# Kernel optimization log

Hardware: AMD Instinct MI355X
Metric: run time of the kernel (lower is better)

Reference implementation:

```python
import jax, jax.numpy as jnp
import numpy as np

# Irrep layout: blocks of (multiplicity, l); identical for input and output.
LS = [0, 1, 2, 3]
MULS = [64, 64, 64, 64]
N = 65536
DIM = sum(m * (2 * l + 1) for m, l in zip(MULS, LS))  # 1024
NPATH = len(LS) * len(LS)  # 16 valid (l_out, l_in) paths
MAXM = max(LS)             # max |m| over all paths
NW = sum(mo * mi for mo in MULS for mi in MULS)  # 65536 path weights


def _split_blocks(x):
    """Split flat irrep vector into per-block [n, mul, 2l+1] views."""
    blocks, off = [], 0
    for mul, l in zip(MULS, LS):
        d = mul * (2 * l + 1)
        blocks.append(x[:, off:off + d].reshape(x.shape[0], mul, 2 * l + 1))
        off += d
    return blocks


def setup_inputs() -> dict:
    key = jax.random.key(0)
    k = jax.random.split(key, 5)
    return {
        "x": jax.random.normal(k[0], (N, DIM), jnp.float32),
        "weights": jax.random.normal(k[1], (NW,), jnp.float32) * 0.1,
        "hzero": jax.random.normal(k[2], (NPATH,), jnp.float32),
        "hpos": jax.random.normal(k[3], (NPATH, MAXM), jnp.float32),
        "hneg": jax.random.normal(k[4], (NPATH, MAXM), jnp.float32),
    }


def reference(x, weights, hzero, hpos, hneg):
    xb = _split_blocks(x)
    n = x.shape[0]
    outb = [jnp.zeros((n, mul, 2 * l + 1), x.dtype) for mul, l in zip(MULS, LS)]
    p, off = 0, 0
    for oi, (mo, lo) in enumerate(zip(MULS, LS)):
        for ii, (mi, li) in enumerate(zip(MULS, LS)):
            W = weights[off:off + mo * mi].reshape(mo, mi)
            off += mo * mi
            xi = xb[ii]  # [n, mi, 2*li+1]
            # m = 0 component
            y0 = jnp.einsum('nm,om->no', xi[:, :, li], W) * hzero[p]
            outb[oi] = outb[oi].at[:, :, lo].add(y0)
            # |m| >= 1: O(2)-reduced pos/neg mixing with Wigner-derived couplings
            for m in range(1, min(lo, li) + 1):
                hp, hn = hpos[p, m - 1], hneg[p, m - 1]
                xp, xn = xi[:, :, li + m], xi[:, :, li - m]
                outb[oi] = outb[oi].at[:, :, lo + m].add(
                    jnp.einsum('nm,om->no', hp * xp + hn * xn, W))
                outb[oi] = outb[oi].at[:, :, lo - m].add(
                    jnp.einsum('nm,om->no', hp * xn - hn * xp, W))
            p += 1
    return jnp.concatenate([b.reshape(n, -1) for b in outb], axis=1)
```

## Files before the change

### kernel.cpp

```cpp
#include <hip/hip_runtime.h>


typedef __attribute__((ext_vector_type(8))) short bhalf8_t;
typedef __attribute__((ext_vector_type(4))) float f32x4_t;

#define NROWS 65536
#define DIMV  1024
#define NT    512
#define RPW   32

#define M0_OFF 0
#define M1_OFF 65536
#define M2_OFF 212992
#define M3_OFF 278528
#define M_TOTAL 294912

#define OP 1028

#define XB1_OFF 11520

__device__ __forceinline__ short f2bf(float f) {
    unsigned u = __builtin_bit_cast(unsigned, f);
    u = (u + 0x7FFFu + ((u >> 16) & 1u)) >> 16;
    return (short)u;
}

__global__ __launch_bounds__(256) void build_M(const float* __restrict__ w,
                                               const float* __restrict__ hz,
                                               const float* __restrict__ hp,
                                               const float* __restrict__ hn,
                                               short* __restrict__ M) {
    int idx = blockIdx.x * 256 + threadIdx.x;
    if (idx >= M_TOTAL) return;

    int m, A, B;
    if (idx < M1_OFF)      { m = 0; int lo = idx;            A = lo / 256u; B = lo - A * 256; }
    else if (idx < M2_OFF) { m = 1; int lo = idx - M1_OFF;   A = lo / 384u; B = lo - A * 384; }
    else if (idx < M3_OFF) { m = 2; int lo = idx - M2_OFF;   A = lo / 256u; B = lo - A * 256; }
    else                   { m = 3; int lo = idx - M3_OFF;   A = lo / 128u; B = lo - A * 128; }

    int ob, so, o, ib, si, i;
    if (m == 0) { ob = A >> 6;       so = 0;            o = A & 63;
                  ib = B >> 6;       si = 0;            i = B & 63; }
    else        { ob = (A >> 7) + m; so = (A >> 6) & 1; o = A & 63;
                  ib = (B >> 7) + m; si = (B >> 6) & 1; i = B & 63; }

    int p = ob * 4 + ib;
    float wv = w[p * 4096 + o * 64 + i];
    float coef;
    if (m == 0) {
        coef = hz[p];
    } else {
        float hpv = hp[p * 3 + (m - 1)];
        float hnv = hn[p * 3 + (m - 1)];
        coef = (so == 0) ? ((si == 0) ? hpv : hnv)
                         : ((si == 0) ? -hnv : hpv);
    }
    M[idx] = f2bf(wv * coef);
}

template<int L>
__device__ __forceinline__ void stage_block(const float* __restrict__ x, int rowbase,
                                            short* __restrict__ xb, int tid) {
    constexpr int nch = 2 * L + 1;
    constexpr int d4  = 16 * nch;
    constexpr int RS  = nch * 72;
    constexpr int bo  = 64 * L * L;
#pragma unroll
    for (int e = 0; e < nch; ++e) {
        int id  = e * NT + tid;
        int row = id / d4;
        int cc  = id - row * d4;
        int col = cc * 4;
        const float4 v = *(const float4*)(x + (size_t)(rowbase + row) * DIMV + bo + col);
        short* dst = &xb[row * RS];
        { int ci = col;     int i = ci / nch; int ji = ci - i * nch; dst[ji * 72 + i] = f2bf(v.x); }
        { int ci = col + 1; int i = ci / nch; int ji = ci - i * nch; dst[ji * 72 + i] = f2bf(v.y); }
        { int ci = col + 2; int i = ci / nch; int ji = ci - i * nch; dst[ji * 72 + i] = f2bf(v.z); }
        { int ci = col + 3; int i = ci / nch; int ji = ci - i * nch; dst[ji * 72 + i] = f2bf(v.w); }
    }
}

template<int L>
__device__ __forceinline__ void compute_block(const short* __restrict__ xb,
                                              const short* __restrict__ Mg,
                                              int m, int Wm, int cb, int lr, int q,
                                              f32x4_t acc[8][2]) {
    if (m > L) return;
    constexpr int nch = 2 * L + 1;
    constexpr int RS  = nch * 72;
    const int nsi = (m == 0) ? 1 : 2;
    for (int si = 0; si < nsi; ++si) {
        const int ji    = L + ((si == 0) ? m : -m);
        const int kbase = (m == 0) ? (L << 6) : (((L - m) << 7) + (si << 6));
#pragma unroll
        for (int kk = 0; kk < 2; ++kk) {
            bhalf8_t a[2];
            const int eo = ji * 72 + kk * 32 + q * 8;
#pragma unroll
            for (int r = 0; r < 2; ++r)
                a[r] = *(const bhalf8_t*)&xb[(r * 16 + lr) * RS + eo];
            const int ko = kbase + kk * 32 + q * 8;
#pragma unroll
            for (int c = 0; c < 8; ++c) {
                const bhalf8_t b = *(const bhalf8_t*)&Mg[(cb + c * 16 + lr) * Wm + ko];
#pragma unroll
                for (int r = 0; r < 2; ++r)
                    acc[c][r] = __builtin_amdgcn_mfma_f32_16x16x32_bf16(
                        a[r], b, acc[c][r], 0, 0, 0);
            }
        }
    }
}

__global__ __launch_bounds__(NT, 4) void tp_main(const float* __restrict__ x,
                                                 const short* __restrict__ Mall,
                                                 float* __restrict__ out) {
    __shared__ __align__(16) char smem[16 * OP * 4];
    short* __restrict__ xb0  = (short*)smem;
    short* __restrict__ xb1  = (short*)smem + XB1_OFF;
    float* __restrict__ obuf = (float*)smem;

    const int tid  = threadIdx.x;
    const int lane = tid & 63;
    const int lr   = lane & 15;
    const int q    = lane >> 4;
    const int wv   = tid >> 6;
    const int rowbase = blockIdx.x * RPW;

    int m, cb;
    if      (wv < 2) { m = 0; cb = wv << 7; }
    else if (wv < 5) { m = 1; cb = (wv - 2) << 7; }
    else if (wv < 7) { m = 2; cb = (wv - 5) << 7; }
    else             { m = 3; cb = 0; }
    const int Wm   = (m == 1) ? 384 : ((m == 3) ? 128 : 256);
    const int Moff = (m == 0) ? M0_OFF : (m == 1) ? M1_OFF : (m == 2) ? M2_OFF : M3_OFF;
    const short* __restrict__ Mg = Mall + Moff;

    f32x4_t acc[8][2];
#pragma unroll
    for (int c = 0; c < 8; ++c)
#pragma unroll
        for (int r = 0; r < 2; ++r)
            acc[c][r] = (f32x4_t){0.f, 0.f, 0.f, 0.f};

    stage_block<0>(x, rowbase, xb0, tid);
    __syncthreads();

    stage_block<1>(x, rowbase, xb1, tid);
    compute_block<0>(xb0, Mg, m, Wm, cb, lr, q, acc);
    __syncthreads();

    stage_block<2>(x, rowbase, xb0, tid);
    compute_block<1>(xb1, Mg, m, Wm, cb, lr, q, acc);
    __syncthreads();

    stage_block<3>(x, rowbase, xb1, tid);
    compute_block<2>(xb0, Mg, m, Wm, cb, lr, q, acc);
    __syncthreads();

    compute_block<3>(xb1, Mg, m, Wm, cb, lr, q, acc);
    __syncthreads();

    int origc[8];
#pragma unroll
    for (int c = 0; c < 8; ++c) {
        const int P = cb + c * 16 + lr;
        int ob, o, jo;
        if (m == 0) { ob = P >> 6;       o = P & 63; jo = ob; }
        else        { ob = (P >> 7) + m; o = P & 63;
                      jo = ob + ((((P >> 6) & 1) == 0) ? m : -m); }
        origc[c] = 64 * ob * ob + o * (2 * ob + 1) + jo;
    }

#pragma unroll
    for (int r2 = 0; r2 < 2; ++r2) {
#pragma unroll
        for (int c = 0; c < 8; ++c) {
#pragma unroll
            for (int g = 0; g < 4; ++g)
                obuf[(q * 4 + g) * OP + origc[c]] = acc[c][r2][g];
        }
        __syncthreads();
#pragma unroll
        for (int it = 0; it < 8; ++it) {
            const int j   = it * NT + tid;
            const int row = j >> 8;
            const int c4  = (j & 255) << 2;
            const float4 v = *(const float4*)&obuf[row * OP + c4];
            *(float4*)&out[(size_t)(rowbase + r2 * 16 + row) * DIMV + c4] = v;
        }
        __syncthreads();
    }
}

extern "C" void kernel_launch(void* const* d_in, const int* in_sizes, int n_in,
                              void* d_out, int out_size, void* d_ws, size_t ws_size,
                              hipStream_t stream) {
    const float* x   = (const float*)d_in[0];
    const float* wts = (const float*)d_in[1];
    const float* hz  = (const float*)d_in[2];
    const float* hp  = (const float*)d_in[3];
    const float* hn  = (const float*)d_in[4];
    float* out = (float*)d_out;
    short* M   = (short*)d_ws;

    build_M<<<dim3(M_TOTAL / 256), dim3(256), 0, stream>>>(wts, hz, hp, hn, M);
    tp_main<<<dim3(NROWS / RPW), dim3(NT), 0, stream>>>(x, M, out);
}
```

Baseline: 583.1 us.

## Double rows per block and prefetch x blocks into registers with single LDS buffer

Each block now handles 64 rows instead of 32, so every M fragment loaded from global memory is reused across four MFMA row tiles instead of two. The LDS double buffer is replaced by a single buffer. The next irrep block of x is loaded into registers while the current block computes, then written to LDS after a barrier. This cuts M reloads per row and keeps global loads overlapped with compute. In exchange it doubles the accumulator registers, lowers the occupancy hint from 4 to 2 blocks per CU, adds barriers, and halves the grid size.

After: 612.8 us. +5.1%, slower.

```diff
diff --git a/kernel.cpp b/kernel.cpp
--- a/kernel.cpp
+++ b/kernel.cpp
@@ -7,7 +7,7 @@
 #define NROWS 65536
 #define DIMV  1024
 #define NT    512
-#define RPW   32
+#define RPW   64
 
 #define M0_OFF 0
 #define M1_OFF 65536
@@ -16,8 +16,6 @@
 #define M_TOTAL 294912
 
 #define OP 1028
-
-#define XB1_OFF 11520
 
 __device__ __forceinline__ short f2bf(float f) {
     unsigned u = __builtin_bit_cast(unsigned, f);
@@ -60,24 +58,38 @@
 }
 
 template<int L>
-__device__ __forceinline__ void stage_block(const float* __restrict__ x, int rowbase,
+__device__ __forceinline__ void load_block(const float* __restrict__ x, int rowbase,
+                                           int tid, float4* __restrict__ v) {
+    constexpr int nch = 2 * L + 1;
+    constexpr int d4  = 16 * nch;
+    constexpr int bo  = 64 * L * L;
+#pragma unroll
+    for (int e = 0; e < 2 * nch; ++e) {
+        int id  = e * NT + tid;
+        int row = id / d4;
+        int cc  = id - row * d4;
+        v[e] = *(const float4*)(x + (size_t)(rowbase + row) * DIMV + bo + cc * 4);
+    }
+}
+
+template<int L>
+__device__ __forceinline__ void write_block(const float4* __restrict__ v,
                                             short* __restrict__ xb, int tid) {
     constexpr int nch = 2 * L + 1;
     constexpr int d4  = 16 * nch;
     constexpr int RS  = nch * 72;
-    constexpr int bo  = 64 * L * L;
-#pragma unroll
-    for (int e = 0; e < nch; ++e) {
+#pragma unroll
+    for (int e = 0; e < 2 * nch; ++e) {
         int id  = e * NT + tid;
         int row = id / d4;
         int cc  = id - row * d4;
         int col = cc * 4;
-        const float4 v = *(const float4*)(x + (size_t)(rowbase + row) * DIMV + bo + col);
         short* dst = &xb[row * RS];
-        { int ci = col;     int i = ci / nch; int ji = ci - i * nch; dst[ji * 72 + i] = f2bf(v.x); }
-        { int ci = col + 1; int i = ci / nch; int ji = ci - i * nch; dst[ji * 72 + i] = f2bf(v.y); }
-        { int ci = col + 2; int i = ci / nch; int ji = ci - i * nch; dst[ji * 72 + i] = f2bf(v.z); }
-        { int ci = col + 3; int i = ci / nch; int ji = ci - i * nch; dst[ji * 72 + i] = f2bf(v.w); }
+        const float4 w = v[e];
+        { int ci = col;     int i = ci / nch; int ji = ci - i * nch; dst[ji * 72 + i] = f2bf(w.x); }
+        { int ci = col + 1; int i = ci / nch; int ji = ci - i * nch; dst[ji * 72 + i] = f2bf(w.y); }
+        { int ci = col + 2; int i = ci / nch; int ji = ci - i * nch; dst[ji * 72 + i] = f2bf(w.z); }
+        { int ci = col + 3; int i = ci / nch; int ji = ci - i * nch; dst[ji * 72 + i] = f2bf(w.w); }
     }
 }
 
@@ -85,7 +97,7 @@
 __device__ __forceinline__ void compute_block(const short* __restrict__ xb,
                                               const short* __restrict__ Mg,
                                               int m, int Wm, int cb, int lr, int q,
-                                              f32x4_t acc[8][2]) {
+                                              f32x4_t (&acc)[8][4]) {
     if (m > L) return;
     constexpr int nch = 2 * L + 1;
     constexpr int RS  = nch * 72;
@@ -95,17 +107,17 @@
         const int kbase = (m == 0) ? (L << 6) : (((L - m) << 7) + (si << 6));
 #pragma unroll
         for (int kk = 0; kk < 2; ++kk) {
-            bhalf8_t a[2];
+            bhalf8_t a[4];
             const int eo = ji * 72 + kk * 32 + q * 8;
 #pragma unroll
-            for (int r = 0; r < 2; ++r)
+            for (int r = 0; r < 4; ++r)
                 a[r] = *(const bhalf8_t*)&xb[(r * 16 + lr) * RS + eo];
             const int ko = kbase + kk * 32 + q * 8;
 #pragma unroll
             for (int c = 0; c < 8; ++c) {
                 const bhalf8_t b = *(const bhalf8_t*)&Mg[(cb + c * 16 + lr) * Wm + ko];
 #pragma unroll
-                for (int r = 0; r < 2; ++r)
+                for (int r = 0; r < 4; ++r)
                     acc[c][r] = __builtin_amdgcn_mfma_f32_16x16x32_bf16(
                         a[r], b, acc[c][r], 0, 0, 0);
             }
@@ -113,12 +125,11 @@
     }
 }
 
-__global__ __launch_bounds__(NT, 4) void tp_main(const float* __restrict__ x,
+__global__ __launch_bounds__(NT, 2) void tp_main(const float* __restrict__ x,
                                                  const short* __restrict__ Mall,
                                                  float* __restrict__ out) {
     __shared__ __align__(16) char smem[16 * OP * 4];
-    short* __restrict__ xb0  = (short*)smem;
-    short* __restrict__ xb1  = (short*)smem + XB1_OFF;
+    short* __restrict__ xbuf = (short*)smem;
     float* __restrict__ obuf = (float*)smem;
 
     const int tid  = threadIdx.x;
@@ -137,30 +148,38 @@
     const int Moff = (m == 0) ? M0_OFF : (m == 1) ? M1_OFF : (m == 2) ? M2_OFF : M3_OFF;
     const short* __restrict__ Mg = Mall + Moff;
 
-    f32x4_t acc[8][2];
+    f32x4_t acc[8][4];
 #pragma unroll
     for (int c = 0; c < 8; ++c)
 #pragma unroll
-        for (int r = 0; r < 2; ++r)
+        for (int r = 0; r < 4; ++r)
             acc[c][r] = (f32x4_t){0.f, 0.f, 0.f, 0.f};
 
-    stage_block<0>(x, rowbase, xb0, tid);
-    __syncthreads();
-
-    stage_block<1>(x, rowbase, xb1, tid);
-    compute_block<0>(xb0, Mg, m, Wm, cb, lr, q, acc);
-    __syncthreads();
-
-    stage_block<2>(x, rowbase, xb0, tid);
-    compute_block<1>(xb1, Mg, m, Wm, cb, lr, q, acc);
-    __syncthreads();
-
-    stage_block<3>(x, rowbase, xb1, tid);
-    compute_block<2>(xb0, Mg, m, Wm, cb, lr, q, acc);
-    __syncthreads();
-
-    compute_block<3>(xb1, Mg, m, Wm, cb, lr, q, acc);
-    __syncthreads();
+    float4 v0[2], v1[6], v2[10], v3[14];
+
+    load_block<0>(x, rowbase, tid, v0);
+    write_block<0>(v0, xbuf, tid);
+    __syncthreads();
+
+    load_block<1>(x, rowbase, tid, v1);
+    compute_block<0>(xbuf, Mg, m, Wm, cb, lr, q, acc);
+    __syncthreads();
+    write_block<1>(v1, xbuf, tid);
+    __syncthreads();
+
+    load_block<2>(x, rowbase, tid, v2);
+    compute_block<1>(xbuf, Mg, m, Wm, cb, lr, q, acc);
+    __syncthreads();
+    write_block<2>(v2, xbuf, tid);
+    __syncthreads();
+
+    load_block<3>(x, rowbase, tid, v3);
+    compute_block<2>(xbuf, Mg, m, Wm, cb, lr, q, acc);
+    __syncthreads();
+    write_block<3>(v3, xbuf, tid);
+    __syncthreads();
+
+    compute_block<3>(xbuf, Mg, m, Wm, cb, lr, q, acc);
 
     int origc[8];
 #pragma unroll
@@ -174,7 +193,8 @@
     }
 
 #pragma unroll
-    for (int r2 = 0; r2 < 2; ++r2) {
+    for (int r2 = 0; r2 < 4; ++r2) {
+        __syncthreads();
 #pragma unroll
         for (int c = 0; c < 8; ++c) {
 #pragma unroll
@@ -190,7 +210,6 @@
             const float4 v = *(const float4*)&obuf[row * OP + c4];
             *(float4*)&out[(size_t)(rowbase + r2 * 16 + row) * DIMV + c4] = v;
         }
-        __syncthreads();
     }
 }
 
```
